# Kernel tuning notes

Hardware: AMD Instinct MI355X
Metric: run time of the kernel (lower is better)

## Reference

```python
import jax, jax.numpy as jnp
import numpy as np

B, D, H, E, C = 16384, 1024, 2048, 4, 3
EPS = 1e-5


def setup_inputs() -> dict:
    key = jax.random.key(0)
    ks = jax.random.split(key, 12)
    s = lambda k, shape, fan: jax.random.normal(k, shape, jnp.float32) * (1.0 / np.sqrt(fan))
    return {
        "x": jax.random.normal(ks[0], (B, D), jnp.float32),
        # gate: LayerNorm(D) -> Linear(D, E)
        "gate_ln_g": jnp.ones((D,), jnp.float32),
        "gate_ln_b": jnp.zeros((D,), jnp.float32),
        "gate_w": s(ks[1], (D, E), D),
        "gate_b": jnp.zeros((E,), jnp.float32),
        # experts (stacked over E): LayerNorm(D) -> Linear(D,H) -> GELU -> Linear(H,C)
        "ex_ln_g": jnp.ones((E, D), jnp.float32),
        "ex_ln_b": jnp.zeros((E, D), jnp.float32),
        "ex_w1": s(ks[2], (E, D, H), D),
        "ex_b1": jnp.zeros((E, H), jnp.float32),
        "ex_w2": s(ks[3], (E, H, C), H),
        "ex_b2": jnp.zeros((E, C), jnp.float32),
    }


def _normalize(x):
    # shared (x - mean) / sqrt(var + eps); per-expert affine applied separately
    mu = jnp.mean(x, axis=-1, keepdims=True)
    var = jnp.mean(jnp.square(x - mu), axis=-1, keepdims=True)
    return (x - mu) * jax.lax.rsqrt(var + EPS)


def reference(x, gate_ln_g, gate_ln_b, gate_w, gate_b,
              ex_ln_g, ex_ln_b, ex_w1, ex_b1, ex_w2, ex_b2):
    normed = _normalize(x)                              # [B, D]
    # gate: LN -> Linear -> softmax over experts
    gate_logits = (normed * gate_ln_g + gate_ln_b) @ gate_w + gate_b   # [B, E]
    gate_weights = jax.nn.softmax(gate_logits, axis=-1)               # [B, E]
    # experts (dropout inactive in eval): per-expert LN affine, MLP with exact GELU
    xn = normed[None, :, :] * ex_ln_g[:, None, :] + ex_ln_b[:, None, :]  # [E, B, D]
    h = jax.nn.gelu(jnp.einsum('ebd,edh->ebh', xn, ex_w1) + ex_b1[:, None, :],
                    approximate=False)                                   # [E, B, H]
    logits = jnp.einsum('ebh,ehc->ebc', h, ex_w2) + ex_b2[:, None, :]    # [E, B, C]
    # gated sum over experts
    return jnp.einsum('be,ebc->bc', gate_weights, logits)               # [B, C]
```

## Files before the change

kernel.cpp:

```cpp
#include <hip/hip_runtime.h>
#include <hip/hip_bf16.h>

typedef __bf16 bf16x8 __attribute__((ext_vector_type(8)));
typedef float  f32x4  __attribute__((ext_vector_type(4)));

__device__ __forceinline__ unsigned short f2bf(float f) {
    union { float f; unsigned int u; } v; v.f = f;
    unsigned int u = v.u;
    unsigned int r = (u + 0x7fffu + ((u >> 16) & 1u)) >> 16;
    return (unsigned short)r;
}

typedef const __attribute__((address_space(1))) unsigned int* gptr_t;
typedef __attribute__((address_space(3))) unsigned int* lptr_t;
__device__ __forceinline__ void async_ld16(const void* g, void* l) {
    __builtin_amdgcn_global_load_lds((gptr_t)g, (lptr_t)l, 16, 0, 0);
}

__device__ __forceinline__ float gelu_fast(float x) {
    const float c1 = 2.30223608f;
    const float c2 = 0.102944903f;
    float s  = x * x;
    float zn = x * __builtin_fmaf(s, -c2, -c1);
    float u  = __builtin_amdgcn_exp2f(zn);
    return x * __builtin_amdgcn_rcpf(1.0f + u);
}

#define Bn 16384
#define Dd 1024
#define Hh 2048
#define Ee 4
#define Cc 3

__global__ void init_b1(const float* __restrict__ b1, float* __restrict__ b1p) {
    int i = blockIdx.x * 256 + threadIdx.x;
    b1p[i] = b1[i];
}

__global__ void prep_w1(const float* __restrict__ w1, const float* __restrict__ exlng,
                        const float* __restrict__ exlnb,
                        unsigned short* __restrict__ w1t, float* __restrict__ b1p) {
    __shared__ float tile[64][65];
    __shared__ float red[4][64];
    const int d0 = blockIdx.x * 64, h0 = blockIdx.y * 64, e = blockIdx.z;
    const int t = threadIdx.x;
    const float* gp = exlng + e * Dd + d0;
    const float* lb = exlnb + e * Dd + d0;
    const float* wp = w1 + ((size_t)e * Dd + d0) * Hh + h0;
    #pragma unroll
    for (int j = 0; j < 16; ++j) {
        int idx = t + j * 256; int dl = idx >> 6, hl = idx & 63;
        tile[dl][hl] = wp[(size_t)dl * Hh + hl];
    }
    __syncthreads();
    #pragma unroll
    for (int j = 0; j < 8; ++j) {
        int idx = t + j * 256; int hl = idx >> 5, k2 = (idx & 31) * 2;
        ushort2 o; o.x = f2bf(tile[k2][hl] * gp[k2]); o.y = f2bf(tile[k2 + 1][hl] * gp[k2 + 1]);
        *(ushort2*)(w1t + ((size_t)(e * Hh + h0 + hl)) * Dd + d0 + k2) = o;
    }
    const int hl = t & 63, dq = t >> 6;
    float acc = 0.f;
    #pragma unroll
    for (int i = 0; i < 16; ++i)
        acc += lb[dq * 16 + i] * tile[dq * 16 + i][hl];
    red[dq][hl] = acc;
    __syncthreads();
    if (t < 64) {
        float s = red[0][t] + red[1][t] + red[2][t] + red[3][t];
        atomicAdd(&b1p[e * Hh + h0 + t], s);
    }
}

__global__ __launch_bounds__(256) void norm_gate(
        const float* __restrict__ x,
        const float* __restrict__ gg, const float* __restrict__ gb,
        const float* __restrict__ gw, const float* __restrict__ gbias,
        unsigned short* __restrict__ normed,
        float* __restrict__ gate) {
    const int row  = blockIdx.x * 4 + (threadIdx.x >> 6);
    const int lane = threadIdx.x & 63;
    const float4* xp = (const float4*)(x + (size_t)row * Dd);
    float4 v[4];
    float s = 0.f, q = 0.f;
    #pragma unroll
    for (int j = 0; j < 4; ++j) {
        v[j] = xp[j * 64 + lane];
        s += v[j].x + v[j].y + v[j].z + v[j].w;
        q += v[j].x * v[j].x + v[j].y * v[j].y + v[j].z * v[j].z + v[j].w * v[j].w;
    }
    #pragma unroll
    for (int off = 32; off; off >>= 1) { s += __shfl_xor(s, off); q += __shfl_xor(q, off); }
    const float mu = s * (1.f / Dd);
    const float var = q * (1.f / Dd) - mu * mu;
    const float rstd = rsqrtf(var + 1e-5f);
    float l0 = 0.f, l1 = 0.f, l2 = 0.f, l3 = 0.f;
    #pragma unroll
    for (int j = 0; j < 4; ++j) {
        const int d = j * 256 + lane * 4;
        float n[4] = { (v[j].x - mu) * rstd, (v[j].y - mu) * rstd,
                       (v[j].z - mu) * rstd, (v[j].w - mu) * rstd };
        ushort4 u; u.x = f2bf(n[0]); u.y = f2bf(n[1]); u.z = f2bf(n[2]); u.w = f2bf(n[3]);
        ((ushort4*)(normed + (size_t)row * Dd))[j * 64 + lane] = u;
        float4 g4 = ((const float4*)gg)[j * 64 + lane];
        float4 b4 = ((const float4*)gb)[j * 64 + lane];
        float a[4] = { n[0] * g4.x + b4.x, n[1] * g4.y + b4.y,
                       n[2] * g4.z + b4.z, n[3] * g4.w + b4.w };
        #pragma unroll
        for (int c = 0; c < 4; ++c) {
            float4 wv = ((const float4*)gw)[d + c];
            l0 += a[c] * wv.x; l1 += a[c] * wv.y; l2 += a[c] * wv.z; l3 += a[c] * wv.w;
        }
    }
    #pragma unroll
    for (int off = 32; off; off >>= 1) {
        l0 += __shfl_xor(l0, off); l1 += __shfl_xor(l1, off);
        l2 += __shfl_xor(l2, off); l3 += __shfl_xor(l3, off);
    }
    if (lane == 0) {
        float L0 = l0 + gbias[0], L1 = l1 + gbias[1], L2 = l2 + gbias[2], L3 = l3 + gbias[3];
        float mx = fmaxf(fmaxf(L0, L1), fmaxf(L2, L3));
        float e0 = expf(L0 - mx), e1 = expf(L1 - mx), e2 = expf(L2 - mx), e3 = expf(L3 - mx);
        float inv = 1.f / (e0 + e1 + e2 + e3);
        float4 gv; gv.x = e0 * inv; gv.y = e1 * inv; gv.z = e2 * inv; gv.w = e3 * inv;
        ((float4*)gate)[row] = gv;
    }
}

__global__ __launch_bounds__(512, 2) void gemm_fused(
    const unsigned short* __restrict__ A,
    const unsigned short* __restrict__ Bt,
    const float* __restrict__ b1p,
    const float* __restrict__ w2,
    float* __restrict__ part)
{
    __shared__ unsigned short As[4][256 * 32];
    __shared__ unsigned short Bs[4][256 * 32];
    __shared__ float w2s[256 * 3];
    __shared__ float b1s[256];

    const int m0 = blockIdx.x * 256;
    const int nb = blockIdx.y;
    const int n0 = nb * 256;
    const int t = threadIdx.x, lane = t & 63, wid = t >> 6;
    const int wm = wid >> 2, wn = wid & 3;
    const int quad = lane >> 4, l15 = lane & 15;

    if (t < 256) {
        b1s[t] = b1p[n0 + t];
        w2s[t * 3 + 0] = w2[(n0 + t) * 3 + 0];
        w2s[t * 3 + 1] = w2[(n0 + t) * 3 + 1];
        w2s[t * 3 + 2] = w2[(n0 + t) * 3 + 2];
    }

    const int srow  = t >> 2;
    const int sslot = (t & 3) ^ ((t >> 3) & 3);
    const unsigned short* ga = A  + (size_t)(m0 + srow) * Dd + sslot * 8;
    const unsigned short* gb = Bt + (size_t)(n0 + srow) * Dd + sslot * 8;
    const int ldoff = t * 8;

#define STAGE_A(kt) { unsigned short* d = &As[(kt) & 3][ldoff];                 \
    async_ld16(ga + (kt) * 32,            d);                                   \
    async_ld16(ga + (kt) * 32 + 128 * Dd, d + 4096); }
#define STAGE_B(kt) { unsigned short* d = &Bs[(kt) & 3][ldoff];                 \
    async_ld16(gb + (kt) * 32,            d);                                   \
    async_ld16(gb + (kt) * 32 + 128 * Dd, d + 4096); }

    f32x4 acc[8][4] = {};

    const int rsw   = (l15 >> 1) & 3;
    const int aBase = (wm * 128 + l15) * 32 + ((quad ^ rsw) * 8);
    const int bBase = (wn * 64  + l15) * 32 + ((quad ^ rsw) * 8);

    STAGE_A(0); STAGE_B(0);
    STAGE_A(1); STAGE_B(1);
    __syncthreads();

    for (int kt = 0; kt < 32; ++kt) {
        const unsigned short* as = &As[kt & 3][0];
        const unsigned short* bs = &Bs[kt & 3][0];

        bf16x8 bf[4], af[8];
        #pragma unroll
        for (int ni = 0; ni < 4; ++ni) bf[ni] = *(const bf16x8*)(bs + bBase + ni * 512);
        #pragma unroll
        for (int mi = 0; mi < 8; ++mi) af[mi] = *(const bf16x8*)(as + aBase + mi * 512);

        if (kt < 30) { STAGE_A(kt + 2); STAGE_B(kt + 2); }

        if (kt < 30) {
            __asm__ volatile("s_waitcnt vmcnt(4)" ::: "memory");
        } else {
            __asm__ volatile("s_waitcnt vmcnt(0)" ::: "memory");
        }
        __builtin_amdgcn_s_barrier();
        __builtin_amdgcn_sched_barrier(0xF);

        __builtin_amdgcn_s_setprio(1);
        #pragma unroll
        for (int mi = 0; mi < 8; ++mi)
            #pragma unroll
            for (int ni = 0; ni < 4; ++ni)
                acc[mi][ni] = __builtin_amdgcn_mfma_f32_16x16x32_bf16(af[mi], bf[ni], acc[mi][ni], 0, 0, 0);
        __builtin_amdgcn_s_setprio(0);
    }
#undef STAGE_A
#undef STAGE_B

    __syncthreads();
    float* redb = (float*)&As[0][0];

    #pragma unroll
    for (int mi = 0; mi < 8; ++mi) {
        float pr[4][3];
        #pragma unroll
        for (int r = 0; r < 4; ++r) { pr[r][0] = 0.f; pr[r][1] = 0.f; pr[r][2] = 0.f; }
        #pragma unroll
        for (int ni = 0; ni < 4; ++ni) {
            const int nl = wn * 64 + ni * 16 + l15;
            const float b1v = b1s[nl];
            const float wa = w2s[nl * 3 + 0], wb = w2s[nl * 3 + 1], wc = w2s[nl * 3 + 2];
            #pragma unroll
            for (int r = 0; r < 4; ++r) {
                float xh = acc[mi][ni][r] + b1v;
                float h = gelu_fast(xh);
                pr[r][0] += h * wa; pr[r][1] += h * wb; pr[r][2] += h * wc;
            }
        }
        #pragma unroll
        for (int off = 1; off < 16; off <<= 1) {
            #pragma unroll
            for (int r = 0; r < 4; ++r) {
                pr[r][0] += __shfl_xor(pr[r][0], off);
                pr[r][1] += __shfl_xor(pr[r][1], off);
                pr[r][2] += __shfl_xor(pr[r][2], off);
            }
        }
        if (l15 == 0) {
            #pragma unroll
            for (int r = 0; r < 4; ++r) {
                const int rl = wm * 128 + mi * 16 + quad * 4 + r;
                float* rb = redb + (rl * 4 + wn) * 3;
                rb[0] = pr[r][0]; rb[1] = pr[r][1]; rb[2] = pr[r][2];
            }
        }
    }
    __syncthreads();
    if (t < 256) {
        const float* rb = redb + t * 12;
        float o0 = rb[0] + rb[3] + rb[6] + rb[9];
        float o1 = rb[1] + rb[4] + rb[7] + rb[10];
        float o2 = rb[2] + rb[5] + rb[8] + rb[11];
        float* pp = part + (size_t)(m0 + t) * 96 + nb * 3;
        pp[0] = o0; pp[1] = o1; pp[2] = o2;
    }
}

__global__ __launch_bounds__(256) void reduce_out(
        const float* __restrict__ part, const float* __restrict__ gate,
        const float* __restrict__ b2, float* __restrict__ out) {
    const int row = blockIdx.x * 256 + threadIdx.x;
    const float4 gv = ((const float4*)gate)[row];
    const float g[4] = { gv.x, gv.y, gv.z, gv.w };
    float o0 = g[0] * b2[0] + g[1] * b2[3] + g[2] * b2[6] + g[3] * b2[9];
    float o1 = g[0] * b2[1] + g[1] * b2[4] + g[2] * b2[7] + g[3] * b2[10];
    float o2 = g[0] * b2[2] + g[1] * b2[5] + g[2] * b2[8] + g[3] * b2[11];
    const float* pp = part + (size_t)row * 96;
    #pragma unroll
    for (int nb = 0; nb < 32; ++nb) {
        const float ge = g[nb >> 3];
        o0 += ge * pp[nb * 3 + 0];
        o1 += ge * pp[nb * 3 + 1];
        o2 += ge * pp[nb * 3 + 2];
    }
    out[row * 3 + 0] = o0; out[row * 3 + 1] = o1; out[row * 3 + 2] = o2;
}

extern "C" void kernel_launch(void* const* d_in, const int* in_sizes, int n_in,
                              void* d_out, int out_size, void* d_ws, size_t ws_size,
                              hipStream_t stream) {
    const float* x     = (const float*)d_in[0];
    const float* gg    = (const float*)d_in[1];
    const float* gb    = (const float*)d_in[2];
    const float* gw    = (const float*)d_in[3];
    const float* gbias = (const float*)d_in[4];
    const float* exlng = (const float*)d_in[5];
    const float* exlnb = (const float*)d_in[6];
    const float* w1    = (const float*)d_in[7];
    const float* b1    = (const float*)d_in[8];
    const float* w2    = (const float*)d_in[9];
    const float* b2    = (const float*)d_in[10];
    float* out = (float*)d_out;

    char* ws = (char*)d_ws;
    unsigned short* normed = (unsigned short*)ws;
    unsigned short* w1t    = (unsigned short*)(ws + 33554432);
    float* b1p  = (float*)(ws + 33554432 + 16777216);
    float* gate = (float*)(ws + 33554432 + 16777216 + 32768);
    float* part = (float*)(ws + 33554432 + 16777216 + 32768 + 262144);

    init_b1<<<32, 256, 0, stream>>>(b1, b1p);
    prep_w1<<<dim3(16, 32, 4), 256, 0, stream>>>(w1, exlng, exlnb, w1t, b1p);
    norm_gate<<<4096, 256, 0, stream>>>(x, gg, gb, gw, gbias, normed, gate);
    gemm_fused<<<dim3(64, 32), 512, 0, stream>>>(normed, w1t, b1p, w2, part);
    reduce_out<<<64, 256, 0, stream>>>(part, gate, b2, out);
}
```

Before: 487.6 us.

## Restructure GEMM main loop to BK=64 double-buffered with interleaved sub-stage loads

Switches the fused GEMM from a 4-deep ring of 32-wide K tiles to two 64-wide K tile buffers, using a matching 8-slot XOR swizzle. Each K iteration is split into four MFMA phases separated by barriers, and each phase issues part of the next tile's async global-to-LDS loads. This halves the loop trip count and spreads load issue across the compute so memory traffic overlaps the matrix math more finely. In exchange it adds extra barriers per iteration and has only one tile in flight, which gives less latency slack than the previous prefetch distance of two.

After: 600.5 us. +23.1%, slower.

```diff
diff --git a/kernel.cpp b/kernel.cpp
--- a/kernel.cpp
+++ b/kernel.cpp
@@ -134,8 +134,8 @@
     const float* __restrict__ w2,
     float* __restrict__ part)
 {
-    __shared__ unsigned short As[4][256 * 32];
-    __shared__ unsigned short Bs[4][256 * 32];
+    __shared__ unsigned short As[2][256 * 64];
+    __shared__ unsigned short Bs[2][256 * 64];
     __shared__ float w2s[256 * 3];
     __shared__ float b1s[256];
 
@@ -153,59 +153,90 @@
         w2s[t * 3 + 2] = w2[(n0 + t) * 3 + 2];
     }
 
-    const int srow  = t >> 2;
-    const int sslot = (t & 3) ^ ((t >> 3) & 3);
+    const int srow  = t >> 3;
+    const int sslot = (t & 7) ^ ((t >> 3) & 7);
     const unsigned short* ga = A  + (size_t)(m0 + srow) * Dd + sslot * 8;
     const unsigned short* gb = Bt + (size_t)(n0 + srow) * Dd + sslot * 8;
-    const int ldoff = t * 8;
-
-#define STAGE_A(kt) { unsigned short* d = &As[(kt) & 3][ldoff];                 \
-    async_ld16(ga + (kt) * 32,            d);                                   \
-    async_ld16(ga + (kt) * 32 + 128 * Dd, d + 4096); }
-#define STAGE_B(kt) { unsigned short* d = &Bs[(kt) & 3][ldoff];                 \
-    async_ld16(gb + (kt) * 32,            d);                                   \
-    async_ld16(gb + (kt) * 32 + 128 * Dd, d + 4096); }
+
+#define STG_A(kt, r0) async_ld16(ga + (size_t)(r0) * Dd + (kt) * 64, \
+                                 &As[(kt) & 1][(r0) * 64 + t * 8])
+#define STG_B(kt, r0) async_ld16(gb + (size_t)(r0) * Dd + (kt) * 64, \
+                                 &Bs[(kt) & 1][(r0) * 64 + t * 8])
 
     f32x4 acc[8][4] = {};
 
-    const int rsw   = (l15 >> 1) & 3;
-    const int aBase = (wm * 128 + l15) * 32 + ((quad ^ rsw) * 8);
-    const int bBase = (wn * 64  + l15) * 32 + ((quad ^ rsw) * 8);
-
-    STAGE_A(0); STAGE_B(0);
-    STAGE_A(1); STAGE_B(1);
-    __syncthreads();
-
-    for (int kt = 0; kt < 32; ++kt) {
-        const unsigned short* as = &As[kt & 3][0];
-        const unsigned short* bs = &Bs[kt & 3][0];
-
-        bf16x8 bf[4], af[8];
-        #pragma unroll
-        for (int ni = 0; ni < 4; ++ni) bf[ni] = *(const bf16x8*)(bs + bBase + ni * 512);
-        #pragma unroll
-        for (int mi = 0; mi < 8; ++mi) af[mi] = *(const bf16x8*)(as + aBase + mi * 512);
-
-        if (kt < 30) { STAGE_A(kt + 2); STAGE_B(kt + 2); }
-
-        if (kt < 30) {
-            __asm__ volatile("s_waitcnt vmcnt(4)" ::: "memory");
-        } else {
-            __asm__ volatile("s_waitcnt vmcnt(0)" ::: "memory");
-        }
+    const int rsw   = l15 & 7;
+    const int aRow  = (wm * 128 + l15) * 64;
+    const int bRow  = (wn * 64  + l15) * 64;
+    const int c0 = ((0 + quad) ^ rsw) * 8;
+    const int c1 = ((4 + quad) ^ rsw) * 8;
+
+    STG_B(0, 0); STG_B(0, 64); STG_B(0, 128); STG_B(0, 192);
+    STG_A(0, 0); STG_A(0, 128);
+    STG_A(0, 64); STG_A(0, 192);
+
+    for (int kt = 0; kt < 16; ++kt) {
+        const unsigned short* as = &As[kt & 1][0];
+        const unsigned short* bs = &Bs[kt & 1][0];
+        bf16x8 bfr[4], af[4];
+
+        __asm__ volatile("s_waitcnt vmcnt(2)" ::: "memory");
         __builtin_amdgcn_s_barrier();
-        __builtin_amdgcn_sched_barrier(0xF);
-
+        if (kt < 15) { STG_B(kt + 1, 0); STG_B(kt + 1, 64); }
+        #pragma unroll
+        for (int ni = 0; ni < 4; ++ni) bfr[ni] = *(const bf16x8*)(bs + bRow + ni * 1024 + c0);
+        #pragma unroll
+        for (int mi = 0; mi < 4; ++mi) af[mi] = *(const bf16x8*)(as + aRow + mi * 1024 + c0);
         __builtin_amdgcn_s_setprio(1);
         #pragma unroll
-        for (int mi = 0; mi < 8; ++mi)
+        for (int mi = 0; mi < 4; ++mi)
             #pragma unroll
             for (int ni = 0; ni < 4; ++ni)
-                acc[mi][ni] = __builtin_amdgcn_mfma_f32_16x16x32_bf16(af[mi], bf[ni], acc[mi][ni], 0, 0, 0);
+                acc[mi][ni] = __builtin_amdgcn_mfma_f32_16x16x32_bf16(af[mi], bfr[ni], acc[mi][ni], 0, 0, 0);
         __builtin_amdgcn_s_setprio(0);
-    }
-#undef STAGE_A
-#undef STAGE_B
+
+        if (kt < 15) { __asm__ volatile("s_waitcnt vmcnt(2)" ::: "memory"); }
+        else         { __asm__ volatile("s_waitcnt vmcnt(0)" ::: "memory"); }
+        __builtin_amdgcn_s_barrier();
+        if (kt < 15) { STG_B(kt + 1, 128); STG_B(kt + 1, 192); }
+        #pragma unroll
+        for (int mi = 0; mi < 4; ++mi) af[mi] = *(const bf16x8*)(as + aRow + 4096 + mi * 1024 + c0);
+        __builtin_amdgcn_s_setprio(1);
+        #pragma unroll
+        for (int mi = 0; mi < 4; ++mi)
+            #pragma unroll
+            for (int ni = 0; ni < 4; ++ni)
+                acc[mi + 4][ni] = __builtin_amdgcn_mfma_f32_16x16x32_bf16(af[mi], bfr[ni], acc[mi + 4][ni], 0, 0, 0);
+        __builtin_amdgcn_s_setprio(0);
+
+        __builtin_amdgcn_s_barrier();
+        if (kt < 15) { STG_A(kt + 1, 0); STG_A(kt + 1, 128); }
+        #pragma unroll
+        for (int ni = 0; ni < 4; ++ni) bfr[ni] = *(const bf16x8*)(bs + bRow + ni * 1024 + c1);
+        #pragma unroll
+        for (int mi = 0; mi < 4; ++mi) af[mi] = *(const bf16x8*)(as + aRow + mi * 1024 + c1);
+        __builtin_amdgcn_s_setprio(1);
+        #pragma unroll
+        for (int mi = 0; mi < 4; ++mi)
+            #pragma unroll
+            for (int ni = 0; ni < 4; ++ni)
+                acc[mi][ni] = __builtin_amdgcn_mfma_f32_16x16x32_bf16(af[mi], bfr[ni], acc[mi][ni], 0, 0, 0);
+        __builtin_amdgcn_s_setprio(0);
+
+        __builtin_amdgcn_s_barrier();
+        if (kt < 15) { STG_A(kt + 1, 64); STG_A(kt + 1, 192); }
+        #pragma unroll
+        for (int mi = 0; mi < 4; ++mi) af[mi] = *(const bf16x8*)(as + aRow + 4096 + mi * 1024 + c1);
+        __builtin_amdgcn_s_setprio(1);
+        #pragma unroll
+        for (int mi = 0; mi < 4; ++mi)
+            #pragma unroll
+            for (int ni = 0; ni < 4; ++ni)
+                acc[mi + 4][ni] = __builtin_amdgcn_mfma_f32_16x16x32_bf16(af[mi], bfr[ni], acc[mi + 4][ni], 0, 0, 0);
+        __builtin_amdgcn_s_setprio(0);
+    }
+#undef STG_A
+#undef STG_B
 
     __syncthreads();
     float* redb = (float*)&As[0][0];
```

## Merge weight prep and norm kernels, drop atomics, remap GEMM blocks per XCD

Applied to the files above, without the earlier changes.

Folds the bias-init, weight-transpose and layernorm/gate kernels into one launch whose blocks take either a norm role or a weight-prep role. The atomic bias accumulation is replaced by per-d-block partial sums that the GEMM reduces when it loads its bias tile. The GEMM grid also becomes 1D with an index remap, so blocks on the same XCD share A row tiles for better L2 reuse. This removes two launches and the atomics, but each GEMM block now does 16 extra strided bias loads.

After: 473.5 us. 2.9% less time.

```diff
diff --git a/kernel.cpp b/kernel.cpp
--- a/kernel.cpp
+++ b/kernel.cpp
@@ -32,105 +32,102 @@
 #define Ee 4
 #define Cc 3
 
-__global__ void init_b1(const float* __restrict__ b1, float* __restrict__ b1p) {
-    int i = blockIdx.x * 256 + threadIdx.x;
-    b1p[i] = b1[i];
-}
-
-__global__ void prep_w1(const float* __restrict__ w1, const float* __restrict__ exlng,
-                        const float* __restrict__ exlnb,
-                        unsigned short* __restrict__ w1t, float* __restrict__ b1p) {
-    __shared__ float tile[64][65];
-    __shared__ float red[4][64];
-    const int d0 = blockIdx.x * 64, h0 = blockIdx.y * 64, e = blockIdx.z;
-    const int t = threadIdx.x;
-    const float* gp = exlng + e * Dd + d0;
-    const float* lb = exlnb + e * Dd + d0;
-    const float* wp = w1 + ((size_t)e * Dd + d0) * Hh + h0;
-    #pragma unroll
-    for (int j = 0; j < 16; ++j) {
-        int idx = t + j * 256; int dl = idx >> 6, hl = idx & 63;
-        tile[dl][hl] = wp[(size_t)dl * Hh + hl];
-    }
-    __syncthreads();
-    #pragma unroll
-    for (int j = 0; j < 8; ++j) {
-        int idx = t + j * 256; int hl = idx >> 5, k2 = (idx & 31) * 2;
-        ushort2 o; o.x = f2bf(tile[k2][hl] * gp[k2]); o.y = f2bf(tile[k2 + 1][hl] * gp[k2 + 1]);
-        *(ushort2*)(w1t + ((size_t)(e * Hh + h0 + hl)) * Dd + d0 + k2) = o;
-    }
-    const int hl = t & 63, dq = t >> 6;
-    float acc = 0.f;
-    #pragma unroll
-    for (int i = 0; i < 16; ++i)
-        acc += lb[dq * 16 + i] * tile[dq * 16 + i][hl];
-    red[dq][hl] = acc;
-    __syncthreads();
-    if (t < 64) {
-        float s = red[0][t] + red[1][t] + red[2][t] + red[3][t];
-        atomicAdd(&b1p[e * Hh + h0 + t], s);
-    }
-}
-
-__global__ __launch_bounds__(256) void norm_gate(
+__global__ __launch_bounds__(256) void prep_and_norm(
         const float* __restrict__ x,
         const float* __restrict__ gg, const float* __restrict__ gb,
         const float* __restrict__ gw, const float* __restrict__ gbias,
-        unsigned short* __restrict__ normed,
-        float* __restrict__ gate) {
-    const int row  = blockIdx.x * 4 + (threadIdx.x >> 6);
-    const int lane = threadIdx.x & 63;
-    const float4* xp = (const float4*)(x + (size_t)row * Dd);
-    float4 v[4];
-    float s = 0.f, q = 0.f;
-    #pragma unroll
-    for (int j = 0; j < 4; ++j) {
-        v[j] = xp[j * 64 + lane];
-        s += v[j].x + v[j].y + v[j].z + v[j].w;
-        q += v[j].x * v[j].x + v[j].y * v[j].y + v[j].z * v[j].z + v[j].w * v[j].w;
-    }
-    #pragma unroll
-    for (int off = 32; off; off >>= 1) { s += __shfl_xor(s, off); q += __shfl_xor(q, off); }
-    const float mu = s * (1.f / Dd);
-    const float var = q * (1.f / Dd) - mu * mu;
-    const float rstd = rsqrtf(var + 1e-5f);
-    float l0 = 0.f, l1 = 0.f, l2 = 0.f, l3 = 0.f;
-    #pragma unroll
-    for (int j = 0; j < 4; ++j) {
-        const int d = j * 256 + lane * 4;
-        float n[4] = { (v[j].x - mu) * rstd, (v[j].y - mu) * rstd,
-                       (v[j].z - mu) * rstd, (v[j].w - mu) * rstd };
-        ushort4 u; u.x = f2bf(n[0]); u.y = f2bf(n[1]); u.z = f2bf(n[2]); u.w = f2bf(n[3]);
-        ((ushort4*)(normed + (size_t)row * Dd))[j * 64 + lane] = u;
-        float4 g4 = ((const float4*)gg)[j * 64 + lane];
-        float4 b4 = ((const float4*)gb)[j * 64 + lane];
-        float a[4] = { n[0] * g4.x + b4.x, n[1] * g4.y + b4.y,
-                       n[2] * g4.z + b4.z, n[3] * g4.w + b4.w };
-        #pragma unroll
-        for (int c = 0; c < 4; ++c) {
-            float4 wv = ((const float4*)gw)[d + c];
-            l0 += a[c] * wv.x; l1 += a[c] * wv.y; l2 += a[c] * wv.z; l3 += a[c] * wv.w;
-        }
-    }
-    #pragma unroll
-    for (int off = 32; off; off >>= 1) {
-        l0 += __shfl_xor(l0, off); l1 += __shfl_xor(l1, off);
-        l2 += __shfl_xor(l2, off); l3 += __shfl_xor(l3, off);
-    }
-    if (lane == 0) {
-        float L0 = l0 + gbias[0], L1 = l1 + gbias[1], L2 = l2 + gbias[2], L3 = l3 + gbias[3];
-        float mx = fmaxf(fmaxf(L0, L1), fmaxf(L2, L3));
-        float e0 = expf(L0 - mx), e1 = expf(L1 - mx), e2 = expf(L2 - mx), e3 = expf(L3 - mx);
-        float inv = 1.f / (e0 + e1 + e2 + e3);
-        float4 gv; gv.x = e0 * inv; gv.y = e1 * inv; gv.z = e2 * inv; gv.w = e3 * inv;
-        ((float4*)gate)[row] = gv;
+        const float* __restrict__ w1, const float* __restrict__ exlng,
+        const float* __restrict__ exlnb,
+        unsigned short* __restrict__ normed, float* __restrict__ gate,
+        unsigned short* __restrict__ w1t, float* __restrict__ b1part) {
+    __shared__ float tile[64][65];
+    __shared__ float red[4][64];
+    const int bid = blockIdx.x, t = threadIdx.x;
+
+    if (bid < 4096) {
+        const int row  = bid * 4 + (t >> 6);
+        const int lane = t & 63;
+        const float4* xp = (const float4*)(x + (size_t)row * Dd);
+        float4 v[4];
+        float s = 0.f, q = 0.f;
+        #pragma unroll
+        for (int j = 0; j < 4; ++j) {
+            v[j] = xp[j * 64 + lane];
+            s += v[j].x + v[j].y + v[j].z + v[j].w;
+            q += v[j].x * v[j].x + v[j].y * v[j].y + v[j].z * v[j].z + v[j].w * v[j].w;
+        }
+        #pragma unroll
+        for (int off = 32; off; off >>= 1) { s += __shfl_xor(s, off); q += __shfl_xor(q, off); }
+        const float mu = s * (1.f / Dd);
+        const float var = q * (1.f / Dd) - mu * mu;
+        const float rstd = rsqrtf(var + 1e-5f);
+        float l0 = 0.f, l1 = 0.f, l2 = 0.f, l3 = 0.f;
+        #pragma unroll
+        for (int j = 0; j < 4; ++j) {
+            const int d = j * 256 + lane * 4;
+            float n[4] = { (v[j].x - mu) * rstd, (v[j].y - mu) * rstd,
+                           (v[j].z - mu) * rstd, (v[j].w - mu) * rstd };
+            ushort4 u; u.x = f2bf(n[0]); u.y = f2bf(n[1]); u.z = f2bf(n[2]); u.w = f2bf(n[3]);
+            ((ushort4*)(normed + (size_t)row * Dd))[j * 64 + lane] = u;
+            float4 g4 = ((const float4*)gg)[j * 64 + lane];
+            float4 b4 = ((const float4*)gb)[j * 64 + lane];
+            float a[4] = { n[0] * g4.x + b4.x, n[1] * g4.y + b4.y,
+                           n[2] * g4.z + b4.z, n[3] * g4.w + b4.w };
+            #pragma unroll
+            for (int c = 0; c < 4; ++c) {
+                float4 wv = ((const float4*)gw)[d + c];
+                l0 += a[c] * wv.x; l1 += a[c] * wv.y; l2 += a[c] * wv.z; l3 += a[c] * wv.w;
+            }
+        }
+        #pragma unroll
+        for (int off = 32; off; off >>= 1) {
+            l0 += __shfl_xor(l0, off); l1 += __shfl_xor(l1, off);
+            l2 += __shfl_xor(l2, off); l3 += __shfl_xor(l3, off);
+        }
+        if (lane == 0) {
+            float L0 = l0 + gbias[0], L1 = l1 + gbias[1], L2 = l2 + gbias[2], L3 = l3 + gbias[3];
+            float mx = fmaxf(fmaxf(L0, L1), fmaxf(L2, L3));
+            float e0 = expf(L0 - mx), e1 = expf(L1 - mx), e2 = expf(L2 - mx), e3 = expf(L3 - mx);
+            float inv = 1.f / (e0 + e1 + e2 + e3);
+            float4 gv; gv.x = e0 * inv; gv.y = e1 * inv; gv.z = e2 * inv; gv.w = e3 * inv;
+            ((float4*)gate)[row] = gv;
+        }
+    } else {
+        const int b2i = bid - 4096;
+        const int d0b = b2i & 15, h0b = (b2i >> 4) & 31, e = b2i >> 9;
+        const int d0 = d0b * 64, h0 = h0b * 64;
+        const float* gp = exlng + e * Dd + d0;
+        const float* lb = exlnb + e * Dd + d0;
+        const float* wp = w1 + ((size_t)e * Dd + d0) * Hh + h0;
+        #pragma unroll
+        for (int j = 0; j < 16; ++j) {
+            int idx = t + j * 256; int dl = idx >> 6, hl = idx & 63;
+            tile[dl][hl] = wp[(size_t)dl * Hh + hl];
+        }
+        __syncthreads();
+        #pragma unroll
+        for (int j = 0; j < 8; ++j) {
+            int idx = t + j * 256; int hl = idx >> 5, k2 = (idx & 31) * 2;
+            ushort2 o; o.x = f2bf(tile[k2][hl] * gp[k2]); o.y = f2bf(tile[k2 + 1][hl] * gp[k2 + 1]);
+            *(ushort2*)(w1t + ((size_t)(e * Hh + h0 + hl)) * Dd + d0 + k2) = o;
+        }
+        const int hl = t & 63, dq = t >> 6;
+        float acc = 0.f;
+        #pragma unroll
+        for (int i = 0; i < 16; ++i)
+            acc += lb[dq * 16 + i] * tile[dq * 16 + i][hl];
+        red[dq][hl] = acc;
+        __syncthreads();
+        if (t < 64)
+            b1part[(size_t)(e * 16 + d0b) * Hh + h0 + t] = red[0][t] + red[1][t] + red[2][t] + red[3][t];
     }
 }
 
 __global__ __launch_bounds__(512, 2) void gemm_fused(
     const unsigned short* __restrict__ A,
     const unsigned short* __restrict__ Bt,
-    const float* __restrict__ b1p,
+    const float* __restrict__ b1,
+    const float* __restrict__ b1part,
     const float* __restrict__ w2,
     float* __restrict__ part)
 {
@@ -139,15 +136,24 @@
     __shared__ float w2s[256 * 3];
     __shared__ float b1s[256];
 
-    const int m0 = blockIdx.x * 256;
-    const int nb = blockIdx.y;
+    const int L = blockIdx.x;
+    const int xcd = L & 7, j = L >> 3;
+    const int mb = (j >> 7) * 32 + xcd * 4 + (j & 3);
+    const int nb = (j >> 2) & 31;
+    const int m0 = mb * 256;
     const int n0 = nb * 256;
+
     const int t = threadIdx.x, lane = t & 63, wid = t >> 6;
     const int wm = wid >> 2, wn = wid & 3;
     const int quad = lane >> 4, l15 = lane & 15;
 
     if (t < 256) {
-        b1s[t] = b1p[n0 + t];
+        const int e = n0 >> 11, hh = n0 & 2047;
+        float s = b1[n0 + t];
+        #pragma unroll
+        for (int i = 0; i < 16; ++i)
+            s += b1part[(size_t)(e * 16 + i) * Hh + hh + t];
+        b1s[t] = s;
         w2s[t * 3 + 0] = w2[(n0 + t) * 3 + 0];
         w2s[t * 3 + 1] = w2[(n0 + t) * 3 + 1];
         w2s[t * 3 + 2] = w2[(n0 + t) * 3 + 2];
@@ -295,13 +301,12 @@
     char* ws = (char*)d_ws;
     unsigned short* normed = (unsigned short*)ws;
     unsigned short* w1t    = (unsigned short*)(ws + 33554432);
-    float* b1p  = (float*)(ws + 33554432 + 16777216);
-    float* gate = (float*)(ws + 33554432 + 16777216 + 32768);
-    float* part = (float*)(ws + 33554432 + 16777216 + 32768 + 262144);
-
-    init_b1<<<32, 256, 0, stream>>>(b1, b1p);
-    prep_w1<<<dim3(16, 32, 4), 256, 0, stream>>>(w1, exlng, exlnb, w1t, b1p);
-    norm_gate<<<4096, 256, 0, stream>>>(x, gg, gb, gw, gbias, normed, gate);
-    gemm_fused<<<dim3(64, 32), 512, 0, stream>>>(normed, w1t, b1p, w2, part);
+    float* b1part = (float*)(ws + 33554432 + 16777216);
+    float* gate   = (float*)(ws + 33554432 + 16777216 + 524288);
+    float* part   = (float*)(ws + 33554432 + 16777216 + 524288 + 262144);
+
+    prep_and_norm<<<6144, 256, 0, stream>>>(x, gg, gb, gw, gbias, w1, exlng, exlnb,
+                                            normed, gate, w1t, b1part);
+    gemm_fused<<<2048, 512, 0, stream>>>(normed, w1t, b1, b1part, w2, part);
     reduce_out<<<64, 256, 0, stream>>>(part, gate, b2, out);
 }
```
